# Performance work log

Hardware: AMD Instinct MI355X
Metric: run time of the kernel (lower is better)

## Reference

```python
import jax, jax.numpy as jnp
import numpy as np

B, S, D = 4, 2048, 1024
H, HD = 16, 64  # num_heads, head_dim
TD = H * HD     # total_dim
SCALE = HD ** -0.5


def setup_inputs() -> dict:
    key = jax.random.key(0)
    ks = jax.random.split(key, 9)
    std = 1.0 / np.sqrt(D)
    return {
        "x": jax.random.normal(ks[0], (B, S, D), dtype=jnp.float32),
        "Wq": jax.random.uniform(ks[1], (D, TD), jnp.float32, -std, std),
        "bq": jax.random.uniform(ks[2], (TD,), jnp.float32, -std, std),
        "Wk": jax.random.uniform(ks[3], (D, TD), jnp.float32, -std, std),
        "bk": jax.random.uniform(ks[4], (TD,), jnp.float32, -std, std),
        "Wv": jax.random.uniform(ks[5], (D, TD), jnp.float32, -std, std),
        "bv": jax.random.uniform(ks[6], (TD,), jnp.float32, -std, std),
        "Wo": jax.random.uniform(ks[7], (TD, D), jnp.float32, -std, std),
        "bo": jax.random.uniform(ks[8], (D,), jnp.float32, -std, std),
    }


def reference(x, Wq, bq, Wk, bk, Wv, bv, Wo, bo):
    # projections -> [B, H, S, HD]
    def split_heads(t):
        return t.reshape(B, S, H, HD).transpose(0, 2, 1, 3)

    q = split_heads(x @ Wq + bq)
    k = split_heads(x @ Wk + bk)
    v = split_heads(x @ Wv + bv)

    # attention scores [B, H, S, S]
    scores = jnp.einsum("bhqd,bhkd->bhqk", q, k) * SCALE
    weights = jax.nn.softmax(scores, axis=-1)
    # dropout is identity in eval mode (p effectively 0)
    attn = jnp.einsum("bhqk,bhkd->bhqd", weights, v)  # [B, H, S, HD]
    attn = attn.transpose(0, 2, 1, 3).reshape(B, S, TD)
    return attn @ Wo + bo
```

## Files before the change

kernel.cpp:

```cpp
#include <hip/hip_runtime.h>
#include <hip/hip_bf16.h>
#include <stdint.h>

#define B_ 4
#define S_ 2048
#define D_ 1024
#define H_ 16
#define HD_ 64
#define TD_ 1024

typedef __attribute__((ext_vector_type(4))) float f32x4;
typedef __attribute__((ext_vector_type(8))) __bf16 bf16x8;
typedef __attribute__((ext_vector_type(4))) __bf16 bf16x4;

__device__ __forceinline__ f32x4 mfma_16x16x32(bf16x8 a, bf16x8 b, f32x4 c) {
  return __builtin_amdgcn_mfma_f32_16x16x32_bf16(a, b, c, 0, 0, 0);
}

__device__ __forceinline__ float fexp2(float x) {
#if __has_builtin(__builtin_amdgcn_exp2f)
  return __builtin_amdgcn_exp2f(x);
#else
  return exp2f(x);
#endif
}

__device__ __forceinline__ uint32_t pkbf16(float lo, float hi) {
  uint32_t r;
  asm("v_cvt_pk_bf16_f32 %0, %1, %2" : "=v"(r) : "v"(lo), "v"(hi));
  return r;
}

__device__ __forceinline__ void gload16(const void* g, void* l) {
  __builtin_amdgcn_global_load_lds(
      (const __attribute__((address_space(1))) uint32_t*)(uintptr_t)g,
      (__attribute__((address_space(3))) uint32_t*)(uintptr_t)l,
      16, 0, 0);
}

__device__ __forceinline__ int xcd_swz(int flat, int nwg) {
  return (flat & 7) * (nwg >> 3) + (flat >> 3);
}


__global__ __launch_bounds__(256) void conv_x_kernel(const float* __restrict__ in,
                                                     __bf16* __restrict__ out) {
  size_t i = ((size_t)blockIdx.x * 256 + threadIdx.x) * 8;
  float4 a = *(const float4*)(in + i);
  float4 b = *(const float4*)(in + i + 4);
  bf16x8 o;
  o[0] = (__bf16)a.x; o[1] = (__bf16)a.y; o[2] = (__bf16)a.z; o[3] = (__bf16)a.w;
  o[4] = (__bf16)b.x; o[5] = (__bf16)b.y; o[6] = (__bf16)b.z; o[7] = (__bf16)b.w;
  *(bf16x8*)(out + i) = o;
}

__global__ __launch_bounds__(256) void wconv4_kernel(
    const float* __restrict__ w0, const float* __restrict__ w1,
    const float* __restrict__ w2, const float* __restrict__ w3,
    __bf16* __restrict__ o0, __bf16* __restrict__ o1,
    __bf16* __restrict__ o2, __bf16* __restrict__ o3, float scale0) {
  const float* in; __bf16* out; float scale;
  switch (blockIdx.z) {
    case 0: in = w0; out = o0; scale = scale0; break;
    case 1: in = w1; out = o1; scale = 1.0f; break;
    case 2: in = w2; out = o2; scale = 1.0f; break;
    default: in = w3; out = o3; scale = 1.0f; break;
  }
  __shared__ float t[64][65];
  const int bx = blockIdx.x * 64;
  const int by = blockIdx.y * 64;
  for (int e = threadIdx.x; e < 4096; e += 256) {
    int r = e >> 6, c = e & 63;
    t[r][c] = in[(size_t)(by + r) * 1024 + bx + c];
  }
  __syncthreads();
  for (int e = threadIdx.x; e < 4096; e += 256) {
    int r = e >> 6, c = e & 63;
    out[(size_t)(bx + r) * 1024 + by + c] = (__bf16)(t[c][r] * scale);
  }
}


#define STG3(SLOT)                                                      \
  gload16(srcA, dstA + (SLOT) * 8192);                                  \
  gload16(srcB, dstB + (SLOT) * 16384);                                 \
  gload16(srcB + 131072, dstB + (SLOT) * 16384 + 8192);                 \
  srcA += 32; srcB += 32;

#define COMPUTE_HALF(SLOT)                                              \
  {                                                                     \
    bf16x8 afr[4], bb[4];                                               \
    _Pragma("unroll") for (int mi = 0; mi < 4; ++mi)                    \
      afr[mi] = *(const bf16x8*)(aptr + (SLOT) * 8192 + mi * 1024);     \
    _Pragma("unroll") for (int ni = 0; ni < 4; ++ni)                    \
      bb[ni] = *(const bf16x8*)(bptr + (SLOT) * 16384 + ni * 1024);     \
    __builtin_amdgcn_s_setprio(1);                                      \
    _Pragma("unroll") for (int mi = 0; mi < 4; ++mi)                    \
      _Pragma("unroll") for (int ni = 0; ni < 4; ++ni)                  \
        acc[mi][ni] = mfma_16x16x32(afr[mi], bb[ni], acc[mi][ni]);      \
    __builtin_amdgcn_s_setprio(0);                                      \
  }

#define BAR_LGKM  asm volatile("s_waitcnt lgkmcnt(0)\n\ts_barrier" ::: "memory")
#define BAR_VM(N) asm volatile("s_waitcnt vmcnt(" #N ")\n\ts_barrier" ::: "memory")
#define BAR_VL(N) asm volatile("s_waitcnt vmcnt(" #N ") lgkmcnt(0)\n\ts_barrier" ::: "memory")

__global__ __launch_bounds__(512, 4) void gemm_qkv3(
    const __bf16* __restrict__ A, const __bf16* __restrict__ Bt,
    const float* __restrict__ bq, const float* __restrict__ bk,
    const float* __restrict__ bv, __bf16* __restrict__ Qout,
    __bf16* __restrict__ Kout, __bf16* __restrict__ Vout, float qscale) {
  __shared__ char SM[73728];
  const int tid = threadIdx.x, lane = tid & 63, wid = tid >> 6;
  const int lrow = lane & 15, g = lane >> 4;
  const int wm = wid >> 2, wn = wid & 3;
  const int flat = blockIdx.y * 12 + blockIdx.x;
  const int swz = xcd_swz(flat, 768);
  const int n0 = (swz % 12) * 256, m0 = (swz / 12) * 128;

  f32x4 acc[4][4];
  const f32x4 zero = {0.f, 0.f, 0.f, 0.f};
#pragma unroll
  for (int i = 0; i < 4; ++i)
#pragma unroll
    for (int j = 0; j < 4; ++j) acc[i][j] = zero;

  const int r0 = tid >> 2, c0 = tid & 3;
  const int csw = c0 ^ ((r0 >> 1) & 3);
  const __bf16* srcA = A + (size_t)(m0 + r0) * 1024 + csw * 8;
  const __bf16* srcB = Bt + (size_t)(n0 + r0) * 1024 + csw * 8;
  char* dstA = SM + wid * 1024;
  char* dstB = SM + 24576 + wid * 1024;

  const int sw = (lrow >> 1) & 3;
  const char* aptr = SM + (wm * 64 + lrow) * 64 + ((g ^ sw) << 4);
  const char* bptr = SM + 24576 + (wn * 64 + lrow) * 64 + ((g ^ sw) << 4);

  STG3(0)
  STG3(1)
  asm volatile("s_waitcnt vmcnt(3)\n\ts_barrier" ::: "memory");

  for (int it = 0; it < 10; ++it) {
    STG3(2)
    COMPUTE_HALF(0)
    BAR_VL(3);
    STG3(0)
    COMPUTE_HALF(1)
    BAR_VL(3);
    STG3(1)
    COMPUTE_HALF(2)
    BAR_VL(3);
  }
  COMPUTE_HALF(0)
  BAR_VL(0);
  COMPUTE_HALF(1)

  const int sel = n0 >> 10;
  if (sel < 2) {
    const float* bias = sel ? bk : bq;
    const float bsc = sel ? 1.0f : qscale;
    __bf16* Out = sel ? Kout : Qout;
#pragma unroll
    for (int mi = 0; mi < 4; ++mi) {
#pragma unroll
      for (int ni = 0; ni < 4; ++ni) {
        const int mbase = m0 + wm * 64 + mi * 16 + g * 4;
        const int nloc = (n0 & 1023) + wn * 64 + ni * 16 + lrow;
        const float bvc = bias[nloc] * bsc;
        const int h = nloc >> 6, hd = nloc & 63;
#pragma unroll
        for (int r = 0; r < 4; ++r) {
          const int m = mbase + r;
          const int b = m >> 11, s = m & 2047;
          Out[((size_t)(b * H_ + h) * S_ + s) * HD_ + hd] = (__bf16)(acc[mi][ni][r] + bvc);
        }
      }
    }
  } else {
#pragma unroll
    for (int mi = 0; mi < 4; ++mi) {
#pragma unroll
      for (int ni = 0; ni < 4; ++ni) {
        const int mbase = m0 + wm * 64 + mi * 16 + g * 4;
        const int t = (n0 & 1023) + wn * 64 + ni * 16 + lrow;
        const float bvc = bv[t];
        bf16x4 w;
#pragma unroll
        for (int r = 0; r < 4; ++r) w[r] = (__bf16)(acc[mi][ni][r] + bvc);
        *(bf16x4*)(Vout + (size_t)t * (B_ * S_) + mbase) = w;
      }
    }
  }
}


#define STG_O(SLOT, KOFF)                                               \
  gload16(srcA + (KOFF), dstA + (SLOT) * 8192);                         \
  gload16(srcA + 65536 + (KOFF), dstA + (SLOT) * 8192 + 4096);          \
  gload16(srcB + (KOFF), dstB + (SLOT) * 8192);                         \
  gload16(srcB + 65536 + (KOFF), dstB + (SLOT) * 8192 + 4096);

#define COMPUTE_O(SLOT)                                                 \
  {                                                                     \
    bf16x8 afr[4], bb[4];                                               \
    _Pragma("unroll") for (int mi = 0; mi < 4; ++mi)                    \
      afr[mi] = *(const bf16x8*)(aptr + (SLOT) * 8192 + mi * 1024);     \
    _Pragma("unroll") for (int ni = 0; ni < 4; ++ni)                    \
      bb[ni] = *(const bf16x8*)(bptr + (SLOT) * 8192 + ni * 1024);      \
    __builtin_amdgcn_s_setprio(1);                                      \
    _Pragma("unroll") for (int mi = 0; mi < 4; ++mi)                    \
      _Pragma("unroll") for (int ni = 0; ni < 4; ++ni)                  \
        acc[mi][ni] = mfma_16x16x32(afr[mi], bb[ni], acc[mi][ni]);      \
    __builtin_amdgcn_s_setprio(0);                                      \
  }

__global__ __launch_bounds__(256, 4) void gemm_out_ring(
    const __bf16* __restrict__ A, const __bf16* __restrict__ Bt,
    const float* __restrict__ bias, float* __restrict__ Cout) {
  __shared__ char SM[32768];
  const int tid = threadIdx.x, lane = tid & 63, wid = tid >> 6;
  const int lrow = lane & 15, g = lane >> 4;
  const int wm = wid >> 1, wn = wid & 1;
  const int flat = blockIdx.y * 8 + blockIdx.x;
  const int swz = xcd_swz(flat, 512);
  const int n0 = (swz & 7) * 128, m0 = (swz >> 3) * 128;

  f32x4 acc[4][4];
  const f32x4 zero = {0.f, 0.f, 0.f, 0.f};
#pragma unroll
  for (int i = 0; i < 4; ++i)
#pragma unroll
    for (int j = 0; j < 4; ++j) acc[i][j] = zero;

  const int r0 = tid >> 2, c0 = tid & 3;
  const int csw = c0 ^ ((r0 >> 1) & 3);
  const __bf16* srcA = A + (size_t)(m0 + r0) * 1024 + csw * 8;
  const __bf16* srcB = Bt + (size_t)(n0 + r0) * 1024 + csw * 8;
  char* dstA = SM + wid * 1024;
  char* dstB = SM + 16384 + wid * 1024;

  const int sw = (lrow >> 1) & 3;
  const char* aptr = SM + (wm * 64 + lrow) * 64 + ((g ^ sw) << 4);
  const char* bptr = SM + 16384 + (wn * 64 + lrow) * 64 + ((g ^ sw) << 4);

  STG_O(0, 0)
  STG_O(1, 32)
  srcA += 64; srcB += 64;
  BAR_VM(4);

  for (int it = 0; it < 15; ++it) {
    COMPUTE_O(0)
    BAR_LGKM;
    STG_O(0, 0)
    BAR_VM(4);
    COMPUTE_O(1)
    BAR_LGKM;
    STG_O(1, 32)
    BAR_VM(4);
    srcA += 64; srcB += 64;
  }
  COMPUTE_O(0)
  BAR_LGKM;
  BAR_VM(0);
  COMPUTE_O(1)

#pragma unroll
  for (int mi = 0; mi < 4; ++mi) {
#pragma unroll
    for (int ni = 0; ni < 4; ++ni) {
      const int mbase = m0 + wm * 64 + mi * 16 + g * 4;
      const int ncol = n0 + wn * 64 + ni * 16 + lrow;
      const float bvc = bias[ncol];
#pragma unroll
      for (int r = 0; r < 4; ++r)
        Cout[(size_t)(mbase + r) * 1024 + ncol] = acc[mi][ni][r] + bvc;
    }
  }
}


__global__ __launch_bounds__(512, 8) void attn_kernel(
    const __bf16* __restrict__ Q, const __bf16* __restrict__ Kp,
    const __bf16* __restrict__ VT, __bf16* __restrict__ O) {
  const int flat = blockIdx.y * gridDim.x + blockIdx.x;
  const int swz = (flat & 7) * 128 + (flat >> 3);
  const int bh = swz >> 4;
  const int q0 = (swz & 15) * 128;
  const int tid = threadIdx.x, lane = tid & 63, wid = tid >> 6;
  const int lrow = lane & 15, g = lane >> 4;
  const int s7 = lrow & 7;
  const int b = bh >> 4, h = bh & 15;

  const __bf16* Qb = Q + (size_t)bh * S_ * HD_;

  __shared__ char SMEM[32768];

  const int qrow = q0 + wid * 16 + lrow;
  const bf16x8 qf0 = *(const bf16x8*)(Qb + (size_t)qrow * HD_ + g * 8);
  const bf16x8 qf1 = *(const bf16x8*)(Qb + (size_t)qrow * HD_ + 32 + g * 8);

  bf16x8 ones;
#pragma unroll
  for (int i = 0; i < 8; ++i) ones[i] = (__bf16)1.0f;

  const int row0 = tid >> 3, sg0 = tid & 7;
  const int kc0 = sg0 ^ (row0 & 7);
  const int kvoff = row0 * HD_ + kc0 * 8;
  const int vvoff = row0 * (B_ * S_) + kc0 * 8;
  const __bf16* Kt = Kp + (size_t)bh * S_ * HD_;
  const __bf16* Vt = VT + (size_t)(h * HD_) * (B_ * S_) + b * S_;
  char* kd0 = SMEM + wid * 1024;
  char* vd0 = SMEM + 16384 + wid * 1024;

  const char* addrA = SMEM + lrow * 128 + ((g ^ s7) << 4);
  const char* addrB = SMEM + lrow * 128 + (((4 + g) ^ s7) << 4);

  f32x4 lacc;
  f32x4 oa[4];
  const f32x4 zero = {0.f, 0.f, 0.f, 0.f};
  const f32x4 minit = {-8.f, -8.f, -8.f, -8.f};
  lacc = zero;
#pragma unroll
  for (int i = 0; i < 4; ++i) oa[i] = zero;

  gload16(Kt + kvoff, kd0);
  gload16(Vt + vvoff, vd0);
  Kt += 64 * HD_; Vt += 64;
  __syncthreads();

  auto stage = [&](const int bo) {
    gload16(Kt + kvoff, kd0 + bo);
    gload16(Vt + vvoff, vd0 + bo);
    Kt += 64 * HD_; Vt += 64;
  };

  auto compute = [&](const int bo) {
    f32x4 sc[4];
    __builtin_amdgcn_s_setprio(1);
#pragma unroll
    for (int kt = 0; kt < 4; ++kt) {
      bf16x8 kf0 = *(const bf16x8*)(addrA + bo + kt * 2048);
      bf16x8 kf1 = *(const bf16x8*)(addrB + bo + kt * 2048);
      f32x4 c = minit;
      c = mfma_16x16x32(kf0, qf0, c);
      c = mfma_16x16x32(kf1, qf1, c);
      sc[kt] = c;
    }
    __builtin_amdgcn_s_setprio(0);

#pragma unroll
    for (int kt = 0; kt < 4; ++kt)
#pragma unroll
      for (int r = 0; r < 4; ++r) sc[kt][r] = fexp2(sc[kt][r]);

    bf16x8 pfrag[2];
#pragma unroll
    for (int s = 0; s < 2; ++s) {
      uint32_t a0 = pkbf16(sc[2 * s][0], sc[2 * s][1]);
      uint32_t a1 = pkbf16(sc[2 * s][2], sc[2 * s][3]);
      uint32_t b0 = pkbf16(sc[2 * s + 1][0], sc[2 * s + 1][1]);
      uint32_t b1 = pkbf16(sc[2 * s + 1][2], sc[2 * s + 1][3]);
      asm volatile("v_permlane32_swap_b32 %0, %1" : "+v"(a0), "+v"(b0));
      asm volatile("v_permlane32_swap_b32 %0, %1" : "+v"(a1), "+v"(b1));
      asm volatile("v_permlane16_swap_b32 %0, %1" : "+v"(a0), "+v"(b0));
      asm volatile("v_permlane16_swap_b32 %0, %1" : "+v"(a1), "+v"(b1));
      union { uint32_t u[4]; bf16x8 v; } pu;
      pu.u[0] = a0; pu.u[1] = a1; pu.u[2] = b0; pu.u[3] = b1;
      pfrag[s] = pu.v;
    }

    __builtin_amdgcn_s_setprio(1);
#pragma unroll
    for (int band = 0; band < 4; ++band) {
      bf16x8 vf0 = *(const bf16x8*)(addrA + 16384 + bo + band * 2048);
      bf16x8 vf1 = *(const bf16x8*)(addrB + 16384 + bo + band * 2048);
      oa[band] = mfma_16x16x32(vf0, pfrag[0], oa[band]);
      oa[band] = mfma_16x16x32(vf1, pfrag[1], oa[band]);
    }
    lacc = mfma_16x16x32(ones, pfrag[0], lacc);
    lacc = mfma_16x16x32(ones, pfrag[1], lacc);
    __builtin_amdgcn_s_setprio(0);
  };

  for (int t = 0; t < S_ / 64; t += 2) {
    stage(8192);
    compute(0);
    __syncthreads();
    if (t + 2 < S_ / 64) stage(0);
    compute(8192);
    __syncthreads();
  }

  const float inv = 1.f / lacc[0];
  __bf16* op = O + ((size_t)(b * S_ + qrow)) * TD_ + h * HD_;
#pragma unroll
  for (int band = 0; band < 4; ++band) {
    bf16x4 w;
#pragma unroll
    for (int r = 0; r < 4; ++r) w[r] = (__bf16)(oa[band][r] * inv);
    *(bf16x4*)(op + band * 16 + g * 4) = w;
  }
}


extern "C" void kernel_launch(void* const* d_in, const int* in_sizes, int n_in,
                              void* d_out, int out_size, void* d_ws, size_t ws_size,
                              hipStream_t stream) {
  const float* x = (const float*)d_in[0];
  const float* Wq = (const float*)d_in[1];
  const float* bq = (const float*)d_in[2];
  const float* Wk = (const float*)d_in[3];
  const float* bk = (const float*)d_in[4];
  const float* Wv = (const float*)d_in[5];
  const float* bv = (const float*)d_in[6];
  const float* Wo = (const float*)d_in[7];
  const float* bo = (const float*)d_in[8];

  char* p = (char*)d_ws;
  const size_t SZ_X = (size_t)B_ * S_ * D_ * 2;
  const size_t SZ_W = (size_t)D_ * TD_ * 2;
  const size_t SZ_QKV = (size_t)B_ * H_ * S_ * HD_ * 2;
  __bf16* xb = (__bf16*)p;  p += SZ_X;
  __bf16* wqT = (__bf16*)p; p += SZ_W;
  __bf16* wkT = (__bf16*)p; p += SZ_W;
  __bf16* wvT = (__bf16*)p; p += SZ_W;
  __bf16* woT = (__bf16*)p; p += SZ_W;
  __bf16* Qb = (__bf16*)p;  p += SZ_QKV;
  __bf16* Kb = (__bf16*)p;  p += SZ_QKV;
  __bf16* VTb = (__bf16*)p; p += SZ_QKV;
  __bf16* attn = xb;

  const float SCALE_Q = 0.125f * 1.4426950408889634f;

  conv_x_kernel<<<4096, 256, 0, stream>>>(x, xb);
  wconv4_kernel<<<dim3(16, 16, 4), 256, 0, stream>>>(Wq, Wk, Wv, Wo,
                                                     wqT, wkT, wvT, woT, SCALE_Q);

  gemm_qkv3<<<dim3(12, 64), 512, 0, stream>>>(
      xb, wqT, bq, bk, bv, Qb, Kb, VTb, SCALE_Q);

  attn_kernel<<<dim3(16, 64), 512, 0, stream>>>(Qb, Kb, VTb, attn);

  gemm_out_ring<<<dim3(8, 64), 256, 0, stream>>>(attn, woT, bo, (float*)d_out);
}
```

Before: 177.6 us.

## Software-pipeline attention loop so PV matmul overlaps next tile's exp

Restructures the attention inner loop so each iteration computes QK^T for the current K tile together with the PV MFMAs for the previous tile's probabilities, then applies exp and packing afterward. V gets a triple-buffered LDS ring (zero-initialized slot for the first iteration) while K stays double-buffered, with a drain step after the loop. The goal is to hide exp/permute latency behind MFMA work. The cost is more LDS (40 KB vs 32 KB), which may reduce occupancy, plus extra live registers for the carried pfrag values.

```diff
diff --git a/kernel.cpp b/kernel.cpp
--- a/kernel.cpp
+++ b/kernel.cpp
@@ -293,7 +293,7 @@
 
   const __bf16* Qb = Q + (size_t)bh * S_ * HD_;
 
-  __shared__ char SMEM[32768];
+  __shared__ char SMEM[40960];
 
   const int qrow = q0 + wid * 16 + lrow;
   const bf16x8 qf0 = *(const bf16x8*)(Qb + (size_t)qrow * HD_ + g * 8);
@@ -309,8 +309,8 @@
   const int vvoff = row0 * (B_ * S_) + kc0 * 8;
   const __bf16* Kt = Kp + (size_t)bh * S_ * HD_;
   const __bf16* Vt = VT + (size_t)(h * HD_) * (B_ * S_) + b * S_;
-  char* kd0 = SMEM + wid * 1024;
-  char* vd0 = SMEM + 16384 + wid * 1024;
+  char* kdst = SMEM + wid * 1024;
+  char* vdst = SMEM + 16384 + wid * 1024;
 
   const char* addrA = SMEM + lrow * 128 + ((g ^ s7) << 4);
   const char* addrB = SMEM + lrow * 128 + (((4 + g) ^ s7) << 4);
@@ -323,37 +323,47 @@
 #pragma unroll
   for (int i = 0; i < 4; ++i) oa[i] = zero;
 
-  gload16(Kt + kvoff, kd0);
-  gload16(Vt + vvoff, vd0);
+  bf16x8 pfrag0, pfrag1;
+#pragma unroll
+  for (int i = 0; i < 8; ++i) { pfrag0[i] = (__bf16)0.0f; pfrag1[i] = (__bf16)0.0f; }
+
+  *(f32x4*)(SMEM + 16384 + 2 * 8192 + tid * 16) = zero;
+
+  gload16(Kt + kvoff, kdst);
+  gload16(Vt + vvoff, vdst);
   Kt += 64 * HD_; Vt += 64;
   __syncthreads();
 
-  auto stage = [&](const int bo) {
-    gload16(Kt + kvoff, kd0 + bo);
-    gload16(Vt + vvoff, vd0 + bo);
-    Kt += 64 * HD_; Vt += 64;
-  };
-
-  auto compute = [&](const int bo) {
+  int kofs = 0;
+  int vprev = 16384, vcur = 0, vnext = 8192;
+
+  auto body = [&](const int ko, const int vp) {
     f32x4 sc[4];
     __builtin_amdgcn_s_setprio(1);
 #pragma unroll
     for (int kt = 0; kt < 4; ++kt) {
-      bf16x8 kf0 = *(const bf16x8*)(addrA + bo + kt * 2048);
-      bf16x8 kf1 = *(const bf16x8*)(addrB + bo + kt * 2048);
+      bf16x8 kf0 = *(const bf16x8*)(addrA + ko + kt * 2048);
+      bf16x8 kf1 = *(const bf16x8*)(addrB + ko + kt * 2048);
       f32x4 c = minit;
       c = mfma_16x16x32(kf0, qf0, c);
       c = mfma_16x16x32(kf1, qf1, c);
       sc[kt] = c;
     }
+#pragma unroll
+    for (int band = 0; band < 4; ++band) {
+      bf16x8 vf0 = *(const bf16x8*)(addrA + 16384 + vp + band * 2048);
+      bf16x8 vf1 = *(const bf16x8*)(addrB + 16384 + vp + band * 2048);
+      oa[band] = mfma_16x16x32(vf0, pfrag0, oa[band]);
+      oa[band] = mfma_16x16x32(vf1, pfrag1, oa[band]);
+    }
+    lacc = mfma_16x16x32(ones, pfrag0, lacc);
+    lacc = mfma_16x16x32(ones, pfrag1, lacc);
     __builtin_amdgcn_s_setprio(0);
 
 #pragma unroll
     for (int kt = 0; kt < 4; ++kt)
 #pragma unroll
       for (int r = 0; r < 4; ++r) sc[kt][r] = fexp2(sc[kt][r]);
-
-    bf16x8 pfrag[2];
 #pragma unroll
     for (int s = 0; s < 2; ++s) {
       uint32_t a0 = pkbf16(sc[2 * s][0], sc[2 * s][1]);
@@ -366,30 +376,31 @@
       asm volatile("v_permlane16_swap_b32 %0, %1" : "+v"(a1), "+v"(b1));
       union { uint32_t u[4]; bf16x8 v; } pu;
       pu.u[0] = a0; pu.u[1] = a1; pu.u[2] = b0; pu.u[3] = b1;
-      pfrag[s] = pu.v;
-    }
-
-    __builtin_amdgcn_s_setprio(1);
-#pragma unroll
-    for (int band = 0; band < 4; ++band) {
-      bf16x8 vf0 = *(const bf16x8*)(addrA + 16384 + bo + band * 2048);
-      bf16x8 vf1 = *(const bf16x8*)(addrB + 16384 + bo + band * 2048);
-      oa[band] = mfma_16x16x32(vf0, pfrag[0], oa[band]);
-      oa[band] = mfma_16x16x32(vf1, pfrag[1], oa[band]);
-    }
-    lacc = mfma_16x16x32(ones, pfrag[0], lacc);
-    lacc = mfma_16x16x32(ones, pfrag[1], lacc);
-    __builtin_amdgcn_s_setprio(0);
+      if (s == 0) pfrag0 = pu.v; else pfrag1 = pu.v;
+    }
   };
 
-  for (int t = 0; t < S_ / 64; t += 2) {
-    stage(8192);
-    compute(0);
+  for (int t = 0; t < 31; ++t) {
+    gload16(Kt + kvoff, kdst + (kofs ^ 8192));
+    gload16(Vt + vvoff, vdst + vnext);
+    Kt += 64 * HD_; Vt += 64;
+    body(kofs, vprev);
     __syncthreads();
-    if (t + 2 < S_ / 64) stage(0);
-    compute(8192);
-    __syncthreads();
-  }
+    kofs ^= 8192;
+    const int tmp = vprev; vprev = vcur; vcur = vnext; vnext = tmp;
+  }
+  body(kofs, vprev);
+  __builtin_amdgcn_s_setprio(1);
+#pragma unroll
+  for (int band = 0; band < 4; ++band) {
+    bf16x8 vf0 = *(const bf16x8*)(addrA + 16384 + vcur + band * 2048);
+    bf16x8 vf1 = *(const bf16x8*)(addrB + 16384 + vcur + band * 2048);
+    oa[band] = mfma_16x16x32(vf0, pfrag0, oa[band]);
+    oa[band] = mfma_16x16x32(vf1, pfrag1, oa[band]);
+  }
+  lacc = mfma_16x16x32(ones, pfrag0, lacc);
+  lacc = mfma_16x16x32(ones, pfrag1, lacc);
+  __builtin_amdgcn_s_setprio(0);
 
   const float inv = 1.f / lacc[0];
   __bf16* op = O + ((size_t)(b * S_ + qrow)) * TD_ + h * HD_;
```

Result: no change. 180.6 us (+1.7%).

## Process two query tiles per wave in attention kernel with 256-thread blocks

Applied to the files above, without the earlier changes.

The attention kernel now runs 4 waves per block instead of 8. Each wave handles 32 query rows as two 16-row sub-tiles that share the same K and V fragments read from LDS. Each thread issues twice as many global-to-LDS loads to fill the same 64-key tile. The aim is to halve LDS fragment reads per MFMA and cut barrier participants, at the cost of higher register pressure and fewer waves per block to hide latency.

```diff
diff --git a/kernel.cpp b/kernel.cpp
--- a/kernel.cpp
+++ b/kernel.cpp
@@ -279,7 +279,7 @@
 }
 
 
-__global__ __launch_bounds__(512, 8) void attn_kernel(
+__global__ __launch_bounds__(256, 4) void attn_kernel(
     const __bf16* __restrict__ Q, const __bf16* __restrict__ Kp,
     const __bf16* __restrict__ VT, __bf16* __restrict__ O) {
   const int flat = blockIdx.y * gridDim.x + blockIdx.x;
@@ -295,15 +295,19 @@
 
   __shared__ char SMEM[32768];
 
-  const int qrow = q0 + wid * 16 + lrow;
-  const bf16x8 qf0 = *(const bf16x8*)(Qb + (size_t)qrow * HD_ + g * 8);
-  const bf16x8 qf1 = *(const bf16x8*)(Qb + (size_t)qrow * HD_ + 32 + g * 8);
+  const int qrowA = q0 + wid * 32 + lrow;
+  const int qrowB = qrowA + 16;
+  const bf16x8 qf0a = *(const bf16x8*)(Qb + (size_t)qrowA * HD_ + g * 8);
+  const bf16x8 qf1a = *(const bf16x8*)(Qb + (size_t)qrowA * HD_ + 32 + g * 8);
+  const bf16x8 qf0b = *(const bf16x8*)(Qb + (size_t)qrowB * HD_ + g * 8);
+  const bf16x8 qf1b = *(const bf16x8*)(Qb + (size_t)qrowB * HD_ + 32 + g * 8);
 
   bf16x8 ones;
 #pragma unroll
   for (int i = 0; i < 8; ++i) ones[i] = (__bf16)1.0f;
 
-  const int row0 = tid >> 3, sg0 = tid & 7;
+  const int gi0 = wid * 64 + lane;
+  const int row0 = gi0 >> 3, sg0 = gi0 & 7;
   const int kc0 = sg0 ^ (row0 & 7);
   const int kvoff = row0 * HD_ + kc0 * 8;
   const int vvoff = row0 * (B_ * S_) + kc0 * 8;
@@ -315,58 +319,81 @@
   const char* addrA = SMEM + lrow * 128 + ((g ^ s7) << 4);
   const char* addrB = SMEM + lrow * 128 + (((4 + g) ^ s7) << 4);
 
-  f32x4 lacc;
-  f32x4 oa[4];
+  f32x4 laccA, laccB;
+  f32x4 oaA[4], oaB[4];
   const f32x4 zero = {0.f, 0.f, 0.f, 0.f};
   const f32x4 minit = {-8.f, -8.f, -8.f, -8.f};
-  lacc = zero;
-#pragma unroll
-  for (int i = 0; i < 4; ++i) oa[i] = zero;
-
-  gload16(Kt + kvoff, kd0);
-  gload16(Vt + vvoff, vd0);
+  laccA = zero; laccB = zero;
+#pragma unroll
+  for (int i = 0; i < 4; ++i) { oaA[i] = zero; oaB[i] = zero; }
+
+  gload16(Kt + kvoff, kd0); gload16(Kt + 32 * HD_ + kvoff, kd0 + 4096);
+  gload16(Vt + vvoff, vd0); gload16(Vt + (size_t)32 * (B_ * S_) + vvoff, vd0 + 4096);
   Kt += 64 * HD_; Vt += 64;
   __syncthreads();
 
   auto stage = [&](const int bo) {
-    gload16(Kt + kvoff, kd0 + bo);
+    gload16(Kt + kvoff, kd0 + bo); gload16(Kt + 32 * HD_ + kvoff, kd0 + bo + 4096);
     gload16(Vt + vvoff, vd0 + bo);
+    gload16(Vt + (size_t)32 * (B_ * S_) + vvoff, vd0 + bo + 4096);
     Kt += 64 * HD_; Vt += 64;
   };
 
   auto compute = [&](const int bo) {
-    f32x4 sc[4];
+    f32x4 sa[4], sb[4];
     __builtin_amdgcn_s_setprio(1);
 #pragma unroll
     for (int kt = 0; kt < 4; ++kt) {
       bf16x8 kf0 = *(const bf16x8*)(addrA + bo + kt * 2048);
       bf16x8 kf1 = *(const bf16x8*)(addrB + bo + kt * 2048);
-      f32x4 c = minit;
-      c = mfma_16x16x32(kf0, qf0, c);
-      c = mfma_16x16x32(kf1, qf1, c);
-      sc[kt] = c;
+      f32x4 ca = minit;
+      ca = mfma_16x16x32(kf0, qf0a, ca);
+      ca = mfma_16x16x32(kf1, qf1a, ca);
+      sa[kt] = ca;
+      f32x4 cb = minit;
+      cb = mfma_16x16x32(kf0, qf0b, cb);
+      cb = mfma_16x16x32(kf1, qf1b, cb);
+      sb[kt] = cb;
     }
     __builtin_amdgcn_s_setprio(0);
 
 #pragma unroll
     for (int kt = 0; kt < 4; ++kt)
 #pragma unroll
-      for (int r = 0; r < 4; ++r) sc[kt][r] = fexp2(sc[kt][r]);
-
-    bf16x8 pfrag[2];
+      for (int r = 0; r < 4; ++r) {
+        sa[kt][r] = fexp2(sa[kt][r]);
+        sb[kt][r] = fexp2(sb[kt][r]);
+      }
+
+    bf16x8 pfa[2], pfb[2];
 #pragma unroll
     for (int s = 0; s < 2; ++s) {
-      uint32_t a0 = pkbf16(sc[2 * s][0], sc[2 * s][1]);
-      uint32_t a1 = pkbf16(sc[2 * s][2], sc[2 * s][3]);
-      uint32_t b0 = pkbf16(sc[2 * s + 1][0], sc[2 * s + 1][1]);
-      uint32_t b1 = pkbf16(sc[2 * s + 1][2], sc[2 * s + 1][3]);
-      asm volatile("v_permlane32_swap_b32 %0, %1" : "+v"(a0), "+v"(b0));
-      asm volatile("v_permlane32_swap_b32 %0, %1" : "+v"(a1), "+v"(b1));
-      asm volatile("v_permlane16_swap_b32 %0, %1" : "+v"(a0), "+v"(b0));
-      asm volatile("v_permlane16_swap_b32 %0, %1" : "+v"(a1), "+v"(b1));
-      union { uint32_t u[4]; bf16x8 v; } pu;
-      pu.u[0] = a0; pu.u[1] = a1; pu.u[2] = b0; pu.u[3] = b1;
-      pfrag[s] = pu.v;
+      {
+        uint32_t a0 = pkbf16(sa[2 * s][0], sa[2 * s][1]);
+        uint32_t a1 = pkbf16(sa[2 * s][2], sa[2 * s][3]);
+        uint32_t b0 = pkbf16(sa[2 * s + 1][0], sa[2 * s + 1][1]);
+        uint32_t b1 = pkbf16(sa[2 * s + 1][2], sa[2 * s + 1][3]);
+        asm volatile("v_permlane32_swap_b32 %0, %1" : "+v"(a0), "+v"(b0));
+        asm volatile("v_permlane32_swap_b32 %0, %1" : "+v"(a1), "+v"(b1));
+        asm volatile("v_permlane16_swap_b32 %0, %1" : "+v"(a0), "+v"(b0));
+        asm volatile("v_permlane16_swap_b32 %0, %1" : "+v"(a1), "+v"(b1));
+        union { uint32_t u[4]; bf16x8 v; } pu;
+        pu.u[0] = a0; pu.u[1] = a1; pu.u[2] = b0; pu.u[3] = b1;
+        pfa[s] = pu.v;
+      }
+      {
+        uint32_t a0 = pkbf16(sb[2 * s][0], sb[2 * s][1]);
+        uint32_t a1 = pkbf16(sb[2 * s][2], sb[2 * s][3]);
+        uint32_t b0 = pkbf16(sb[2 * s + 1][0], sb[2 * s + 1][1]);
+        uint32_t b1 = pkbf16(sb[2 * s + 1][2], sb[2 * s + 1][3]);
+        asm volatile("v_permlane32_swap_b32 %0, %1" : "+v"(a0), "+v"(b0));
+        asm volatile("v_permlane32_swap_b32 %0, %1" : "+v"(a1), "+v"(b1));
+        asm volatile("v_permlane16_swap_b32 %0, %1" : "+v"(a0), "+v"(b0));
+        asm volatile("v_permlane16_swap_b32 %0, %1" : "+v"(a1), "+v"(b1));
+        union { uint32_t u[4]; bf16x8 v; } pu;
+        pu.u[0] = a0; pu.u[1] = a1; pu.u[2] = b0; pu.u[3] = b1;
+        pfb[s] = pu.v;
+      }
     }
 
     __builtin_amdgcn_s_setprio(1);
@@ -374,11 +401,15 @@
     for (int band = 0; band < 4; ++band) {
       bf16x8 vf0 = *(const bf16x8*)(addrA + 16384 + bo + band * 2048);
       bf16x8 vf1 = *(const bf16x8*)(addrB + 16384 + bo + band * 2048);
-      oa[band] = mfma_16x16x32(vf0, pfrag[0], oa[band]);
-      oa[band] = mfma_16x16x32(vf1, pfrag[1], oa[band]);
-    }
-    lacc = mfma_16x16x32(ones, pfrag[0], lacc);
-    lacc = mfma_16x16x32(ones, pfrag[1], lacc);
+      oaA[band] = mfma_16x16x32(vf0, pfa[0], oaA[band]);
+      oaA[band] = mfma_16x16x32(vf1, pfa[1], oaA[band]);
+      oaB[band] = mfma_16x16x32(vf0, pfb[0], oaB[band]);
+      oaB[band] = mfma_16x16x32(vf1, pfb[1], oaB[band]);
+    }
+    laccA = mfma_16x16x32(ones, pfa[0], laccA);
+    laccA = mfma_16x16x32(ones, pfa[1], laccA);
+    laccB = mfma_16x16x32(ones, pfb[0], laccB);
+    laccB = mfma_16x16x32(ones, pfb[1], laccB);
     __builtin_amdgcn_s_setprio(0);
   };
 
@@ -391,14 +422,20 @@
     __syncthreads();
   }
 
-  const float inv = 1.f / lacc[0];
-  __bf16* op = O + ((size_t)(b * S_ + qrow)) * TD_ + h * HD_;
+  const float invA = 1.f / laccA[0];
+  const float invB = 1.f / laccB[0];
+  __bf16* opA = O + ((size_t)(b * S_ + qrowA)) * TD_ + h * HD_;
+  __bf16* opB = O + ((size_t)(b * S_ + qrowB)) * TD_ + h * HD_;
 #pragma unroll
   for (int band = 0; band < 4; ++band) {
-    bf16x4 w;
-#pragma unroll
-    for (int r = 0; r < 4; ++r) w[r] = (__bf16)(oa[band][r] * inv);
-    *(bf16x4*)(op + band * 16 + g * 4) = w;
+    bf16x4 wa, wb;
+#pragma unroll
+    for (int r = 0; r < 4; ++r) {
+      wa[r] = (__bf16)(oaA[band][r] * invA);
+      wb[r] = (__bf16)(oaB[band][r] * invB);
+    }
+    *(bf16x4*)(opA + band * 16 + g * 4) = wa;
+    *(bf16x4*)(opB + band * 16 + g * 4) = wb;
   }
 }
 
@@ -439,7 +476,7 @@
   gemm_qkv3<<<dim3(12, 64), 512, 0, stream>>>(
       xb, wqT, bq, bk, bv, Qb, Kb, VTb, SCALE_Q);
 
-  attn_kernel<<<dim3(16, 64), 512, 0, stream>>>(Qb, Kb, VTb, attn);
+  attn_kernel<<<dim3(16, 64), 256, 0, stream>>>(Qb, Kb, VTb, attn);
 
   gemm_out_ring<<<dim3(8, 64), 256, 0, stream>>>(attn, woT, bo, (float*)d_out);
 }
```

Result: faster. 172.4 us (-3.0%).
